# Kernel tuning notes

Hardware: AMD Instinct MI355X
Metric: run time of the kernel (lower is better)

Reference implementation:

```python
import jax, jax.numpy as jnp
import numpy as np
from functools import partial

B, DIN, H, D, HW = 4096, 2048, 1024, 256, 256
MAX_STEPS = 15
STEP = 1.0 / MAX_STEPS
WEIGHT = 1.0


def safe_norm(x):
    # per-sample L2 norm, keepdims, nan-safe at 0
    return jnp.sqrt(jnp.sum(x * x, axis=-1, keepdims=True) + 1e-24)


def setup_inputs() -> dict:
    key = jax.random.key(0)
    ks = jax.random.split(key, 16)
    s = lambda fan: 1.0 / np.sqrt(fan)
    inp = {
        'x_start': jax.random.normal(ks[0], (B, DIN), jnp.float32),
        'x_end': jax.random.normal(ks[1], (B, DIN), jnp.float32),
        'noise_raw': jax.random.normal(ks[2], (B, D), jnp.float32),
        # encoder params
        'W1': jax.random.normal(ks[3], (DIN, H), jnp.float32) * s(DIN),
        'b1': jnp.zeros((H,), jnp.float32),
        'W2': jax.random.normal(ks[4], (H, D), jnp.float32) * s(H),
        'b2': jnp.zeros((D,), jnp.float32),
        # Zermelo wind field params
        'Ww1': jax.random.normal(ks[5], (D, HW), jnp.float32) * s(D),
        'bw1': jnp.zeros((HW,), jnp.float32),
        'Ww2': jax.random.normal(ks[6], (HW, D), jnp.float32) * s(HW),
        'bw2': jnp.zeros((D,), jnp.float32),
        # conformal potential phi params (metric g = exp(phi) I)
        'Wp1': jax.random.normal(ks[7], (D, HW), jnp.float32) * s(D),
        'bp1': jnp.zeros((HW,), jnp.float32),
        'wp2': jax.random.normal(ks[8], (HW,), jnp.float32) * s(HW),
    }
    return inp


def _encode(x, W1, b1, W2, b2):
    return jnp.tanh(x @ W1 + b1) @ W2 + b2  # [B, D]


def _wind(z, Ww1, bw1, Ww2, bw2):
    return jnp.tanh(z @ Ww1 + bw1) @ Ww2 + bw2  # [B, D]


def _grad_phi(x, Wp1, bp1, wp2):
    # phi(x) = wp2 . tanh(x @ Wp1 + bp1); analytic gradient, fully vectorized
    h = jnp.tanh(x @ Wp1 + bp1)          # [B, HW]
    return ((1.0 - h * h) * wp2) @ Wp1.T  # [B, D]


def _accel(x, v, Wp1, bp1, wp2):
    # geodesic spray of conformal metric e^{phi} I:
    # a = -(grad_phi . v) v + 0.5 |v|^2 grad_phi
    g = _grad_phi(x, Wp1, bp1, wp2)
    gv = jnp.sum(g * v, axis=-1, keepdims=True)
    vv = jnp.sum(v * v, axis=-1, keepdims=True)
    return -gv * v + 0.5 * vv * g


def _trace(z0, v0, Wp1, bp1, wp2):
    h = STEP
    acc = partial(_accel, Wp1=Wp1, bp1=bp1, wp2=wp2)

    def step(carry, _):
        x, v = carry
        k1x, k1v = v, acc(x, v)
        k2x, k2v = v + 0.5 * h * k1v, acc(x + 0.5 * h * k1x, v + 0.5 * h * k1v)
        k3x, k3v = v + 0.5 * h * k2v, acc(x + 0.5 * h * k2x, v + 0.5 * h * k2v)
        k4x, k4v = v + h * k3v, acc(x + h * k3x, v + h * k3v)
        xn = x + (h / 6.0) * (k1x + 2 * k2x + 2 * k3x + k4x)
        vn = v + (h / 6.0) * (k1v + 2 * k2v + 2 * k3v + k4v)
        return (xn, vn), xn

    (_, _), xs = jax.lax.scan(step, (z0, v0), None, length=MAX_STEPS)
    return xs  # [MAX_STEPS, B, D] == xs[1:] of the original trace


def reference(x_start, x_end, noise_raw, W1, b1, W2, b2,
              Ww1, bw1, Ww2, bw2, Wp1, bp1, wp2):
    z_s = _encode(x_start, W1, b1, W2, b2)
    z_e = _encode(x_end, W1, b1, W2, b2)
    W_start = _wind(z_s, Ww1, bw1, Ww2, bw2)
    # degenerate-wind fallback: tiny tangent noise (Euclidean manifold -> identity projection)
    noise = noise_raw / (safe_norm(noise_raw) + 1e-12) * 1e-4
    w_norm = safe_norm(W_start)  # [B, 1]
    W_start = jnp.where(w_norm < 1e-5, W_start + noise, W_start)
    xs = _trace(z_s, W_start, Wp1, bp1, wp2)          # [S, B, D]
    dists_sq = jnp.sum((xs - z_e) ** 2, axis=-1)      # [S, B]
    min_dist_sq = jnp.min(dists_sq, axis=0)           # closest approach per sample
    return jnp.mean(min_dist_sq) * WEIGHT
```

## Files before the change

kernel.cpp:

```cpp
#include <hip/hip_runtime.h>
#include <math.h>

typedef short bf8 __attribute__((ext_vector_type(8)));
typedef float f32x4 __attribute__((ext_vector_type(4)));

namespace {

constexpr float H_STEP = 1.0f / 15.0f;

__device__ inline short f2bf(float f) {
  unsigned u = __float_as_uint(f);
  u += 0x7fffu + ((u >> 16) & 1u);
  return (short)(u >> 16);
}

__device__ inline float fast_tanh(float x) {
  const float ax = fabsf(x);
  const float e = __expf(-2.0f * ax);
  const float t = (1.0f - e) * __builtin_amdgcn_rcpf(1.0f + e);
  return copysignf(t, x);
}

__device__ inline float sech2(float x) {
  const float e = __expf(-2.0f * fabsf(x));
  const float r = __builtin_amdgcn_rcpf(1.0f + e);
  return 4.0f * e * r * r;
}

__device__ inline float wave_sum(float v) {
#pragma unroll
  for (int sh = 32; sh > 0; sh >>= 1) v += __shfl_xor(v, sh);
  return v;
}

template <int CTRL>
__device__ inline float dppadd(float v) {
  return v + __int_as_float(__builtin_amdgcn_update_dpp(
                 0, __float_as_int(v), CTRL, 0xF, 0xF, true));
}
__device__ inline float red16(float v) {
  v = dppadd<0x121>(v);
  v = dppadd<0x122>(v);
  v = dppadd<0x124>(v);
  v = dppadd<0x128>(v);
  return v;
}

__device__ inline void async16(const void* g, void* l) {
  __builtin_amdgcn_global_load_lds((__attribute__((address_space(1))) void*)g,
                                   (__attribute__((address_space(3))) void*)l,
                                   16, 0, 0);
}

__global__ __launch_bounds__(256) void prep_all(
    const float* __restrict__ xs, const float* __restrict__ xe,
    const float* __restrict__ W1, const float* __restrict__ W2,
    const float* __restrict__ Ww1, const float* __restrict__ Ww2,
    const float* __restrict__ Wp1, const float* __restrict__ wp2,
    short* __restrict__ XSb, short* __restrict__ W1T, short* __restrict__ W2T,
    short* __restrict__ Ww1T, short* __restrict__ Ww2T,
    short* __restrict__ WpT, short* __restrict__ Wp1s) {
  __shared__ float tile[32][33];
  const int id = blockIdx.x;
  if (id < 2048) {
    const long n = (long)8192 * 2048, half = n >> 1;
    long i = ((long)id * 256 + threadIdx.x) * 4;
    const long stride = (long)2048 * 1024;
    for (; i < n; i += stride) {
      const float* s = (i < half) ? (xs + i) : (xe + (i - half));
      const float4 f = *(const float4*)s;
      ushort4 o;
      o.x = (unsigned short)f2bf(f.x);
      o.y = (unsigned short)f2bf(f.y);
      o.z = (unsigned short)f2bf(f.z);
      o.w = (unsigned short)f2bf(f.w);
      *(ushort4*)(XSb + i) = o;
    }
    return;
  }
  const int tr = threadIdx.x >> 5, tc = threadIdx.x & 31;
  const float* src;
  short* dst;
  int K, N, kt, nt;
  if (id < 4096) {
    src = W1; dst = W1T; K = 2048; N = 1024; kt = (id - 2048) >> 5; nt = (id - 2048) & 31;
  } else if (id < 4352) {
    src = W2; dst = W2T; K = 1024; N = 256; kt = (id - 4096) >> 3; nt = (id - 4096) & 7;
  } else if (id < 4416) {
    src = Ww1; dst = Ww1T; K = 256; N = 256; kt = (id - 4352) >> 3; nt = (id - 4352) & 7;
  } else if (id < 4480) {
    src = Ww2; dst = Ww2T; K = 256; N = 256; kt = (id - 4416) >> 3; nt = (id - 4416) & 7;
  } else if (id < 4544) {
    src = Wp1; dst = WpT; K = 256; N = 256; kt = (id - 4480) >> 3; nt = (id - 4480) & 7;
  } else {
    const int lid = id - 4544;
    const int k0 = (lid >> 3) * 32, n0 = (lid & 7) * 32;
#pragma unroll
    for (int i = 0; i < 32; i += 8) {
      const size_t o = (size_t)(k0 + tr + i) * 256 + n0 + tc;
      Wp1s[o] = f2bf(Wp1[o] * wp2[n0 + tc]);
    }
    return;
  }
  const int k0 = kt * 32, n0 = nt * 32;
#pragma unroll
  for (int i = 0; i < 32; i += 8)
    tile[tr + i][tc] = src[(size_t)(k0 + tr + i) * N + n0 + tc];
  __syncthreads();
#pragma unroll
  for (int i = 0; i < 32; i += 8)
    dst[(size_t)(n0 + tr + i) * K + k0 + tc] = f2bf(tile[tc][tr + i]);
}


__global__ __launch_bounds__(256) void gemm128_tanh(
    const short* __restrict__ A, const short* __restrict__ Bt,
    const float* __restrict__ bias, short* __restrict__ Cb, int M, int N,
    int K) {
  __shared__ __align__(16) short As[2 * 128 * 32];
  __shared__ __align__(16) short Bs[2 * 128 * 32];
  const int tid = threadIdx.x;
  const int w = tid >> 6, lane = tid & 63, q = lane >> 4, l15 = lane & 15;
  const int wm = (w >> 1) * 64, wn = (w & 1) * 64;
  const int m0 = blockIdx.y * 128, n0 = blockIdx.x * 128;
  const f32x4 fzero = {0.0f, 0.0f, 0.0f, 0.0f};
  f32x4 acc[4][4];
#pragma unroll
  for (int mt = 0; mt < 4; ++mt)
#pragma unroll
    for (int nt = 0; nt < 4; ++nt) acc[mt][nt] = fzero;

  for (int k0 = 0; k0 < K; k0 += 64) {
#pragma unroll
    for (int kcb = 0; kcb < 2; ++kcb)
#pragma unroll
      for (int j = 0; j < 2; ++j) {
        const int c = w * 128 + j * 64 + lane;
        async16(A + (size_t)(m0 + (c >> 2)) * K + k0 + kcb * 32 + (c & 3) * 8,
                &As[kcb * 4096 + (w * 128 + j * 64) * 8]);
        async16(Bt + (size_t)(n0 + (c >> 2)) * K + k0 + kcb * 32 + (c & 3) * 8,
                &Bs[kcb * 4096 + (w * 128 + j * 64) * 8]);
      }
    __syncthreads();
#pragma unroll
    for (int kcb = 0; kcb < 2; ++kcb) {
      bf8 af[4], bfr[4];
#pragma unroll
      for (int mt = 0; mt < 4; ++mt)
        af[mt] =
            *(const bf8*)&As[kcb * 4096 + (wm + mt * 16 + l15) * 32 + q * 8];
#pragma unroll
      for (int nt = 0; nt < 4; ++nt)
        bfr[nt] =
            *(const bf8*)&Bs[kcb * 4096 + (wn + nt * 16 + l15) * 32 + q * 8];
#pragma unroll
      for (int mt = 0; mt < 4; ++mt)
#pragma unroll
        for (int nt = 0; nt < 4; ++nt)
          acc[mt][nt] = __builtin_amdgcn_mfma_f32_16x16x32_bf16(
              af[mt], bfr[nt], acc[mt][nt], 0, 0, 0);
    }
    __syncthreads();
  }
#pragma unroll
  for (int mt = 0; mt < 4; ++mt)
#pragma unroll
    for (int nt = 0; nt < 4; ++nt) {
      const int col = n0 + wn + nt * 16 + l15;
      const float bcol = bias[col];
#pragma unroll
      for (int rg = 0; rg < 4; ++rg) {
        const int row = m0 + wm + mt * 16 + q * 4 + rg;
        Cb[(size_t)row * N + col] = f2bf(fast_tanh(acc[mt][nt][rg] + bcol));
      }
    }
}

__global__ __launch_bounds__(256) void gemm64_enc2(
    const short* __restrict__ A, const short* __restrict__ Bt,
    const float* __restrict__ bias, float* __restrict__ Zs,
    float* __restrict__ Ze, int M, int N, int K) {
  __shared__ __align__(16) short As[2 * 64 * 32];
  __shared__ __align__(16) short Bs[2 * 64 * 32];
  const int tid = threadIdx.x;
  const int w = tid >> 6, lane = tid & 63, q = lane >> 4, l15 = lane & 15;
  const int wm = (w >> 1) * 32, wn = (w & 1) * 32;
  const int m0 = blockIdx.y * 64, n0 = blockIdx.x * 64;
  const f32x4 fzero = {0.0f, 0.0f, 0.0f, 0.0f};
  f32x4 acc[2][2];
#pragma unroll
  for (int mt = 0; mt < 2; ++mt)
#pragma unroll
    for (int nt = 0; nt < 2; ++nt) acc[mt][nt] = fzero;

  for (int k0 = 0; k0 < K; k0 += 64) {
    const int c = w * 64 + lane;
#pragma unroll
    for (int kcb = 0; kcb < 2; ++kcb) {
      async16(A + (size_t)(m0 + (c >> 2)) * K + k0 + kcb * 32 + (c & 3) * 8,
              &As[kcb * 2048 + (w * 64) * 8]);
      async16(Bt + (size_t)(n0 + (c >> 2)) * K + k0 + kcb * 32 + (c & 3) * 8,
              &Bs[kcb * 2048 + (w * 64) * 8]);
    }
    __syncthreads();
#pragma unroll
    for (int kcb = 0; kcb < 2; ++kcb) {
      bf8 af[2], bfr[2];
#pragma unroll
      for (int mt = 0; mt < 2; ++mt)
        af[mt] =
            *(const bf8*)&As[kcb * 2048 + (wm + mt * 16 + l15) * 32 + q * 8];
#pragma unroll
      for (int nt = 0; nt < 2; ++nt)
        bfr[nt] =
            *(const bf8*)&Bs[kcb * 2048 + (wn + nt * 16 + l15) * 32 + q * 8];
#pragma unroll
      for (int mt = 0; mt < 2; ++mt)
#pragma unroll
        for (int nt = 0; nt < 2; ++nt)
          acc[mt][nt] = __builtin_amdgcn_mfma_f32_16x16x32_bf16(
              af[mt], bfr[nt], acc[mt][nt], 0, 0, 0);
    }
    __syncthreads();
  }
#pragma unroll
  for (int mt = 0; mt < 2; ++mt)
#pragma unroll
    for (int nt = 0; nt < 2; ++nt) {
      const int col = n0 + wn + nt * 16 + l15;
      const float bcol = bias[col];
#pragma unroll
      for (int rg = 0; rg < 4; ++rg) {
        const int row = m0 + wm + mt * 16 + q * 4 + rg;
        const float val = acc[mt][nt][rg] + bcol;
        if (row < 4096)
          Zs[(size_t)row * N + col] = val;
        else
          Ze[(size_t)(row - 4096) * N + col] = val;
      }
    }
}


__global__ __launch_bounds__(512, 2) void trace_fused(
    const float* __restrict__ Xg, const float* __restrict__ ZEg,
    const float* __restrict__ NZg, const short* __restrict__ WT,
    const short* __restrict__ Wp1s, const short* __restrict__ Ww1T,
    const short* __restrict__ Ww2T, const float* __restrict__ bw1,
    const float* __restrict__ bw2, const float* __restrict__ bp1,
    float* __restrict__ out) {
  constexpr float hs = H_STEP;
  __shared__ __align__(16) short XsL[4096];
  __shared__ __align__(16) short UL[4096];
  __shared__ __align__(16) float gvb[2][16];
  __shared__ __align__(16) float vvb[2][16];
  __shared__ __align__(16) float db[2][16];
  const int tid = threadIdx.x;
  const int w = tid >> 6, lane = tid & 63, q = lane >> 4, l15 = lane & 15;
  const int r0 = blockIdx.x * 16, rb = q * 4;

  if (tid < 16) {
    gvb[0][tid] = 0.0f; gvb[1][tid] = 0.0f;
    vvb[0][tid] = 0.0f; vvb[1][tid] = 0.0f;
    db[0][tid] = 0.0f;  db[1][tid] = 0.0f;
  }

  int cc[2], wadr[2][4], radr[8];
  float bp1c[2], bw1c[2], bw2c[2];
#pragma unroll
  for (int t = 0; t < 2; ++t) {
    const int c = w * 32 + t * 16 + l15;
    cc[t] = c;
    const int kc = c >> 3, cx = kc & 15, cl = c & 7;
#pragma unroll
    for (int rg = 0; rg < 4; ++rg)
      wadr[t][rg] = kc * 128 + ((rb + rg) ^ cx) * 8 + cl;
    bp1c[t] = bp1[c];
    bw1c[t] = bw1[c];
    bw2c[t] = bw2[c];
  }
#pragma unroll
  for (int ks = 0; ks < 8; ++ks) {
    const int kq = ks * 4 + q;
    radr[ks] = (kq * 16 + (l15 ^ (kq & 15))) * 8;
  }
  float x[2][4], ze[2][4], nz[2][4];
#pragma unroll
  for (int t = 0; t < 2; ++t)
#pragma unroll
    for (int rg = 0; rg < 4; ++rg) {
      const size_t off = (size_t)(r0 + rb + rg) * 256 + cc[t];
      x[t][rg] = Xg[off];
      ze[t][rg] = ZEg[off];
      nz[t][rg] = NZg[off];
    }
  const f32x4 fzero = {0.0f, 0.0f, 0.0f, 0.0f};

  float v[2][4];
  {
    bf8 Wf1[2][8], Wf2[2][8];
#pragma unroll
    for (int t = 0; t < 2; ++t)
#pragma unroll
      for (int ks = 0; ks < 8; ++ks) {
        Wf1[t][ks] = *(const bf8*)(Ww1T + cc[t] * 256 + ks * 32 + q * 8);
        Wf2[t][ks] = *(const bf8*)(Ww2T + cc[t] * 256 + ks * 32 + q * 8);
      }
#pragma unroll
    for (int t = 0; t < 2; ++t)
#pragma unroll
      for (int rg = 0; rg < 4; ++rg) XsL[wadr[t][rg]] = f2bf(x[t][rg]);
    __syncthreads();
    bf8 af[8];
#pragma unroll
    for (int ks = 0; ks < 8; ++ks) af[ks] = *(const bf8*)&XsL[radr[ks]];
    f32x4 acc[2];
#pragma unroll
    for (int t = 0; t < 2; ++t) {
      f32x4 a0 = fzero, a1 = fzero;
#pragma unroll
      for (int ks = 0; ks < 8; ks += 2) {
        a0 = __builtin_amdgcn_mfma_f32_16x16x32_bf16(af[ks], Wf1[t][ks], a0,
                                                     0, 0, 0);
        a1 = __builtin_amdgcn_mfma_f32_16x16x32_bf16(af[ks + 1],
                                                     Wf1[t][ks + 1], a1, 0, 0,
                                                     0);
      }
      acc[t] = a0 + a1;
    }
#pragma unroll
    for (int t = 0; t < 2; ++t)
#pragma unroll
      for (int rg = 0; rg < 4; ++rg)
        UL[wadr[t][rg]] = f2bf(fast_tanh(acc[t][rg] + bw1c[t]));
    __syncthreads();
#pragma unroll
    for (int ks = 0; ks < 8; ++ks) af[ks] = *(const bf8*)&UL[radr[ks]];
#pragma unroll
    for (int t = 0; t < 2; ++t) {
      f32x4 a0 = fzero, a1 = fzero;
#pragma unroll
      for (int ks = 0; ks < 8; ks += 2) {
        a0 = __builtin_amdgcn_mfma_f32_16x16x32_bf16(af[ks], Wf2[t][ks], a0,
                                                     0, 0, 0);
        a1 = __builtin_amdgcn_mfma_f32_16x16x32_bf16(af[ks + 1],
                                                     Wf2[t][ks + 1], a1, 0, 0,
                                                     0);
      }
      acc[t] = a0 + a1;
#pragma unroll
      for (int rg = 0; rg < 4; ++rg) v[t][rg] = acc[t][rg] + bw2c[t];
    }
    float pn[4], pm[4];
#pragma unroll
    for (int rg = 0; rg < 4; ++rg) {
      pn[rg] = red16(v[0][rg] * v[0][rg] + v[1][rg] * v[1][rg]);
      pm[rg] = red16(nz[0][rg] * nz[0][rg] + nz[1][rg] * nz[1][rg]);
    }
    if (l15 == 0) {
#pragma unroll
      for (int rg = 0; rg < 4; ++rg) {
        atomicAdd(&gvb[0][rb + rg], pn[rg]);
        atomicAdd(&vvb[0][rb + rg], pm[rg]);
      }
    }
    __syncthreads();
#pragma unroll
    for (int rg = 0; rg < 4; ++rg) {
      const float wn = sqrtf(gvb[0][rb + rg] + 1e-24f);
      const float sc = (wn < 1e-5f)
                           ? 1e-4f / (sqrtf(vvb[0][rb + rg] + 1e-24f) + 1e-12f)
                           : 0.0f;
      v[0][rg] = fmaf(sc, nz[0][rg], v[0][rg]);
      v[1][rg] = fmaf(sc, nz[1][rg], v[1][rg]);
    }
    __syncthreads();
    if (tid < 16) {
      gvb[0][tid] = 0.0f;
      vvb[0][tid] = 0.0f;
    }
    __syncthreads();
  }

  bf8 B1f[2][8], B2f[2][8];
#pragma unroll
  for (int t = 0; t < 2; ++t)
#pragma unroll
    for (int ks = 0; ks < 8; ++ks) {
      B1f[t][ks] = *(const bf8*)(WT + cc[t] * 256 + ks * 32 + q * 8);
      B2f[t][ks] = *(const bf8*)(Wp1s + cc[t] * 256 + ks * 32 + q * 8);
    }
  float ap[2][4], xacc[2][4], vacc[2][4], md[4];
#pragma unroll
  for (int rg = 0; rg < 4; ++rg) {
    ap[0][rg] = 0.0f; ap[1][rg] = 0.0f;
    xacc[0][rg] = 0.0f; xacc[1][rg] = 0.0f;
    vacc[0][rg] = 0.0f; vacc[1][rg] = 0.0f;
    md[rg] = 3.4e38f;
  }
  const float cxv_t[4] = {0.0f, 0.5f * hs, 0.5f * hs, hs};
  const float cxa_t[4] = {0.0f, 0.0f, 0.25f * hs * hs, 0.5f * hs * hs};
  const float cva_t[4] = {0.0f, 0.5f * hs, 0.5f * hs, hs};

#pragma unroll 1
  for (int step = 0; step < 15; ++step) {
#pragma unroll
    for (int st = 0; st < 4; ++st) {
      const int p = st & 1;
      const float cxv = cxv_t[st], cxa = cxa_t[st], cva = cva_t[st];
      float vs[2][4];
#pragma unroll
      for (int t = 0; t < 2; ++t)
#pragma unroll
        for (int rg = 0; rg < 4; ++rg) {
          vs[t][rg] = fmaf(cva, ap[t][rg], v[t][rg]);
          XsL[wadr[t][rg]] =
              f2bf(x[t][rg] + cxv * v[t][rg] + cxa * ap[t][rg]);
        }
      {
        float pv[4];
#pragma unroll
        for (int rg = 0; rg < 4; ++rg)
          pv[rg] = red16(fmaf(vs[0][rg], vs[0][rg], vs[1][rg] * vs[1][rg]));
        if (l15 == 0) {
#pragma unroll
          for (int rg = 0; rg < 4; ++rg) atomicAdd(&vvb[p][rb + rg], pv[rg]);
        }
      }
      __syncthreads();
      if (st == 0 && step > 0) {
        const f32x4 d4 = *(const f32x4*)&db[(step - 1) & 1][rb];
#pragma unroll
        for (int rg = 0; rg < 4; ++rg) md[rg] = fminf(md[rg], d4[rg]);
      }
      bf8 af[8];
#pragma unroll
      for (int ks = 0; ks < 8; ++ks) af[ks] = *(const bf8*)&XsL[radr[ks]];
      f32x4 acc[2];
#pragma unroll
      for (int t = 0; t < 2; ++t) {
        f32x4 a0 = fzero, a1 = fzero;
#pragma unroll
        for (int ks = 0; ks < 8; ks += 2) {
          a0 = __builtin_amdgcn_mfma_f32_16x16x32_bf16(af[ks], B1f[t][ks], a0,
                                                       0, 0, 0);
          a1 = __builtin_amdgcn_mfma_f32_16x16x32_bf16(af[ks + 1],
                                                       B1f[t][ks + 1], a1, 0,
                                                       0, 0);
        }
        acc[t] = a0 + a1;
      }
#pragma unroll
      for (int t = 0; t < 2; ++t)
#pragma unroll
        for (int rg = 0; rg < 4; ++rg)
          UL[wadr[t][rg]] = f2bf(sech2(acc[t][rg] + bp1c[t]));
      if (tid < 16) {
        gvb[p ^ 1][tid] = 0.0f;
        vvb[p ^ 1][tid] = 0.0f;
      }
      __syncthreads();
      if (st == 0 && step > 0 && tid < 16) db[(step - 1) & 1][tid] = 0.0f;
#pragma unroll
      for (int ks = 0; ks < 8; ++ks) af[ks] = *(const bf8*)&UL[radr[ks]];
#pragma unroll
      for (int t = 0; t < 2; ++t) {
        f32x4 a0 = fzero, a1 = fzero;
#pragma unroll
        for (int ks = 0; ks < 8; ks += 2) {
          a0 = __builtin_amdgcn_mfma_f32_16x16x32_bf16(af[ks], B2f[t][ks], a0,
                                                       0, 0, 0);
          a1 = __builtin_amdgcn_mfma_f32_16x16x32_bf16(af[ks + 1],
                                                       B2f[t][ks + 1], a1, 0,
                                                       0, 0);
        }
        acc[t] = a0 + a1;
      }
      {
        float pg[4];
#pragma unroll
        for (int rg = 0; rg < 4; ++rg)
          pg[rg] =
              red16(fmaf(acc[0][rg], vs[0][rg], acc[1][rg] * vs[1][rg]));
        if (l15 == 0) {
#pragma unroll
          for (int rg = 0; rg < 4; ++rg) atomicAdd(&gvb[p][rb + rg], pg[rg]);
        }
      }
      __syncthreads();
      const f32x4 gv4 = *(const f32x4*)&gvb[p][rb];
      const f32x4 vv4 = *(const f32x4*)&vvb[p][rb];
#pragma unroll
      for (int t = 0; t < 2; ++t)
#pragma unroll
        for (int rg = 0; rg < 4; ++rg) {
          const float a = -gv4[rg] * vs[t][rg] + 0.5f * vv4[rg] * acc[t][rg];
          ap[t][rg] = a;
          if (st == 0) {
            xacc[t][rg] = a;
            vacc[t][rg] = a;
          } else if (st < 3) {
            xacc[t][rg] += a;
            vacc[t][rg] += 2.0f * a;
          } else {
            vacc[t][rg] += a;
          }
        }
      if (st == 3) {
        const int sp = step & 1;
        float pd[4];
#pragma unroll
        for (int rg = 0; rg < 4; ++rg) {
          float acc_d = 0.0f;
#pragma unroll
          for (int t = 0; t < 2; ++t) {
            const float xn =
                x[t][rg] + hs * v[t][rg] + (hs * hs / 6.0f) * xacc[t][rg];
            const float vn = v[t][rg] + (hs / 6.0f) * vacc[t][rg];
            x[t][rg] = xn;
            v[t][rg] = vn;
            const float d = xn - ze[t][rg];
            acc_d = fmaf(d, d, acc_d);
          }
          pd[rg] = red16(acc_d);
        }
        if (l15 == 0) {
#pragma unroll
          for (int rg = 0; rg < 4; ++rg) atomicAdd(&db[sp][rb + rg], pd[rg]);
        }
      }
    }
  }
  __syncthreads();
  {
    const f32x4 d4 = *(const f32x4*)&db[14 & 1][rb];
#pragma unroll
    for (int rg = 0; rg < 4; ++rg) md[rg] = fminf(md[rg], d4[rg]);
  }
  if (w == 0 && l15 == 0)
    atomicAdd(out, (md[0] + md[1] + md[2] + md[3]) * (1.0f / 4096.0f));
}

}

extern "C" void kernel_launch(void* const* d_in, const int* in_sizes, int n_in,
                              void* d_out, int out_size, void* d_ws,
                              size_t ws_size, hipStream_t stream) {
  (void)in_sizes; (void)n_in; (void)out_size; (void)ws_size;
  const float* x_start = (const float*)d_in[0];
  const float* x_end = (const float*)d_in[1];
  const float* noise = (const float*)d_in[2];
  const float* W1 = (const float*)d_in[3];
  const float* b1 = (const float*)d_in[4];
  const float* W2 = (const float*)d_in[5];
  const float* b2 = (const float*)d_in[6];
  const float* Ww1 = (const float*)d_in[7];
  const float* bw1 = (const float*)d_in[8];
  const float* Ww2 = (const float*)d_in[9];
  const float* bw2 = (const float*)d_in[10];
  const float* Wp1 = (const float*)d_in[11];
  const float* bp1 = (const float*)d_in[12];
  const float* wp2 = (const float*)d_in[13];
  float* out = (float*)d_out;

  float* Xf = (float*)d_ws;
  float* ZEf = Xf + (size_t)4096 * 256;
  short* XSb = (short*)(ZEf + (size_t)4096 * 256);
  short* H1b = XSb + (size_t)8192 * 2048;
  short* W1T = H1b + (size_t)8192 * 1024;
  short* W2T = W1T + (size_t)1024 * 2048;
  short* Ww1T = W2T + (size_t)256 * 1024;
  short* Ww2T = Ww1T + 65536;
  short* WpT = Ww2T + 65536;
  short* Wp1s = WpT + 65536;

  const dim3 blk(256);

  prep_all<<<4608, blk, 0, stream>>>(x_start, x_end, W1, W2, Ww1, Ww2, Wp1,
                                     wp2, XSb, W1T, W2T, Ww1T, Ww2T, WpT,
                                     Wp1s);
  gemm128_tanh<<<dim3(8, 64), blk, 0, stream>>>(XSb, W1T, b1, H1b, 8192, 1024,
                                                2048);
  gemm64_enc2<<<dim3(4, 128), blk, 0, stream>>>(H1b, W2T, b2, Xf, ZEf, 8192,
                                                256, 1024);
  hipMemsetAsync(d_out, 0, sizeof(float), stream);
  trace_fused<<<256, dim3(512), 0, stream>>>(Xf, ZEf, noise, WpT, Wp1s, Ww1T,
                                             Ww2T, bw1, bw2, bp1, out);
}
```

Baseline: 326.5 us.

## Transpose MFMA operands in trace kernel so each lane owns one row's columns

```diff
diff --git a/kernel.cpp b/kernel.cpp
--- a/kernel.cpp
+++ b/kernel.cpp
@@ -2,6 +2,7 @@
 #include <math.h>
 
 typedef short bf8 __attribute__((ext_vector_type(8)));
+typedef short s4v __attribute__((ext_vector_type(4)));
 typedef float f32x4 __attribute__((ext_vector_type(4)));
 
 namespace {
@@ -25,12 +26,6 @@
   const float e = __expf(-2.0f * fabsf(x));
   const float r = __builtin_amdgcn_rcpf(1.0f + e);
   return 4.0f * e * r * r;
-}
-
-__device__ inline float wave_sum(float v) {
-#pragma unroll
-  for (int sh = 32; sh > 0; sh >>= 1) v += __shfl_xor(v, sh);
-  return v;
 }
 
 template <int CTRL>
@@ -50,6 +45,16 @@
   __builtin_amdgcn_global_load_lds((__attribute__((address_space(1))) void*)g,
                                    (__attribute__((address_space(3))) void*)l,
                                    16, 0, 0);
+}
+
+__device__ inline void stpk4(short* base, int byteoff, float a, float b,
+                             float c, float d) {
+  s4v s;
+  s[0] = f2bf(a);
+  s[1] = f2bf(b);
+  s[2] = f2bf(c);
+  s[3] = f2bf(d);
+  *(s4v*)((char*)base + byteoff) = s;
 }
 
 __global__ __launch_bounds__(256) void prep_all(
@@ -59,10 +64,12 @@
     const float* __restrict__ Wp1, const float* __restrict__ wp2,
     short* __restrict__ XSb, short* __restrict__ W1T, short* __restrict__ W2T,
     short* __restrict__ Ww1T, short* __restrict__ Ww2T,
-    short* __restrict__ WpT, short* __restrict__ Wp1s) {
+    short* __restrict__ WpT, short* __restrict__ Wp1s,
+    float* __restrict__ outz) {
   __shared__ float tile[32][33];
   const int id = blockIdx.x;
   if (id < 2048) {
+    if (id == 0 && threadIdx.x == 0) *outz = 0.0f;
     const long n = (long)8192 * 2048, half = n >> 1;
     long i = ((long)id * 256 + threadIdx.x) * 4;
     const long stride = (long)2048 * 1024;
@@ -252,48 +259,49 @@
   constexpr float hs = H_STEP;
   __shared__ __align__(16) short XsL[4096];
   __shared__ __align__(16) short UL[4096];
-  __shared__ __align__(16) float gvb[2][16];
-  __shared__ __align__(16) float vvb[2][16];
+  __shared__ __align__(16) float gvv[2][16][2];
   __shared__ __align__(16) float db[2][16];
   const int tid = threadIdx.x;
   const int w = tid >> 6, lane = tid & 63, q = lane >> 4, l15 = lane & 15;
-  const int r0 = blockIdx.x * 16, rb = q * 4;
+  const int r0 = blockIdx.x * 16;
+  const int col0 = w * 32 + q * 4;
+  const int wrow = w * 32 + l15;
 
   if (tid < 16) {
-    gvb[0][tid] = 0.0f; gvb[1][tid] = 0.0f;
-    vvb[0][tid] = 0.0f; vvb[1][tid] = 0.0f;
-    db[0][tid] = 0.0f;  db[1][tid] = 0.0f;
-  }
-
-  int cc[2], wadr[2][4], radr[8];
-  float bp1c[2], bw1c[2], bw2c[2];
+    *(float2*)gvv[0][tid] = make_float2(0.f, 0.f);
+    *(float2*)gvv[1][tid] = make_float2(0.f, 0.f);
+    db[0][tid] = 0.f;
+    db[1][tid] = 0.f;
+  }
+
+  const int smask = ((l15 & 7) << 2) ^ (l15 & 3);
+  int wadrT[2], radrT[8];
 #pragma unroll
   for (int t = 0; t < 2; ++t) {
-    const int c = w * 32 + t * 16 + l15;
-    cc[t] = c;
-    const int kc = c >> 3, cx = kc & 15, cl = c & 7;
-#pragma unroll
-    for (int rg = 0; rg < 4; ++rg)
-      wadr[t][rg] = kc * 128 + ((rb + rg) ^ cx) * 8 + cl;
-    bp1c[t] = bp1[c];
-    bw1c[t] = bw1[c];
-    bw2c[t] = bw2[c];
-  }
-#pragma unroll
-  for (int ks = 0; ks < 8; ++ks) {
-    const int kq = ks * 4 + q;
-    radr[ks] = (kq * 16 + (l15 ^ (kq & 15))) * 8;
-  }
+    const int slot = w * 4 + t * 2 + (q >> 1);
+    wadrT[t] = (l15 * 32 + (slot ^ smask)) * 16 + (q & 1) * 8;
+  }
+#pragma unroll
+  for (int ks = 0; ks < 8; ++ks)
+    radrT[ks] = (l15 * 32 + ((ks * 4 + q) ^ smask)) * 16;
+
   float x[2][4], ze[2][4], nz[2][4];
 #pragma unroll
-  for (int t = 0; t < 2; ++t)
-#pragma unroll
-    for (int rg = 0; rg < 4; ++rg) {
-      const size_t off = (size_t)(r0 + rb + rg) * 256 + cc[t];
-      x[t][rg] = Xg[off];
-      ze[t][rg] = ZEg[off];
-      nz[t][rg] = NZg[off];
-    }
+  for (int t = 0; t < 2; ++t) {
+    const size_t off = (size_t)(r0 + l15) * 256 + col0 + t * 16;
+    const float4 xa = *(const float4*)(Xg + off);
+    const float4 za = *(const float4*)(ZEg + off);
+    const float4 na = *(const float4*)(NZg + off);
+    x[t][0] = xa.x; x[t][1] = xa.y; x[t][2] = xa.z; x[t][3] = xa.w;
+    ze[t][0] = za.x; ze[t][1] = za.y; ze[t][2] = za.z; ze[t][3] = za.w;
+    nz[t][0] = na.x; nz[t][1] = na.y; nz[t][2] = na.z; nz[t][3] = na.w;
+  }
+  float bp1c[2][4];
+#pragma unroll
+  for (int t = 0; t < 2; ++t) {
+    const float4 pa = *(const float4*)(bp1 + col0 + t * 16);
+    bp1c[t][0] = pa.x; bp1c[t][1] = pa.y; bp1c[t][2] = pa.z; bp1c[t][3] = pa.w;
+  }
   const f32x4 fzero = {0.0f, 0.0f, 0.0f, 0.0f};
 
   float v[2][4];
@@ -303,82 +311,90 @@
     for (int t = 0; t < 2; ++t)
 #pragma unroll
       for (int ks = 0; ks < 8; ++ks) {
-        Wf1[t][ks] = *(const bf8*)(Ww1T + cc[t] * 256 + ks * 32 + q * 8);
-        Wf2[t][ks] = *(const bf8*)(Ww2T + cc[t] * 256 + ks * 32 + q * 8);
-      }
+        Wf1[t][ks] =
+            *(const bf8*)(Ww1T + (size_t)(wrow + t * 16) * 256 + ks * 32 + q * 8);
+        Wf2[t][ks] =
+            *(const bf8*)(Ww2T + (size_t)(wrow + t * 16) * 256 + ks * 32 + q * 8);
+      }
+    float bw1c[2][4], bw2c[2][4];
+#pragma unroll
+    for (int t = 0; t < 2; ++t) {
+      const float4 a1 = *(const float4*)(bw1 + col0 + t * 16);
+      const float4 a2 = *(const float4*)(bw2 + col0 + t * 16);
+      bw1c[t][0] = a1.x; bw1c[t][1] = a1.y; bw1c[t][2] = a1.z; bw1c[t][3] = a1.w;
+      bw2c[t][0] = a2.x; bw2c[t][1] = a2.y; bw2c[t][2] = a2.z; bw2c[t][3] = a2.w;
+    }
 #pragma unroll
     for (int t = 0; t < 2; ++t)
-#pragma unroll
-      for (int rg = 0; rg < 4; ++rg) XsL[wadr[t][rg]] = f2bf(x[t][rg]);
+      stpk4(XsL, wadrT[t], x[t][0], x[t][1], x[t][2], x[t][3]);
     __syncthreads();
     bf8 af[8];
 #pragma unroll
-    for (int ks = 0; ks < 8; ++ks) af[ks] = *(const bf8*)&XsL[radr[ks]];
+    for (int ks = 0; ks < 8; ++ks)
+      af[ks] = *(const bf8*)((const char*)XsL + radrT[ks]);
     f32x4 acc[2];
 #pragma unroll
     for (int t = 0; t < 2; ++t) {
       f32x4 a0 = fzero, a1 = fzero;
 #pragma unroll
       for (int ks = 0; ks < 8; ks += 2) {
-        a0 = __builtin_amdgcn_mfma_f32_16x16x32_bf16(af[ks], Wf1[t][ks], a0,
-                                                     0, 0, 0);
-        a1 = __builtin_amdgcn_mfma_f32_16x16x32_bf16(af[ks + 1],
-                                                     Wf1[t][ks + 1], a1, 0, 0,
-                                                     0);
+        a0 = __builtin_amdgcn_mfma_f32_16x16x32_bf16(Wf1[t][ks], af[ks], a0, 0,
+                                                     0, 0);
+        a1 = __builtin_amdgcn_mfma_f32_16x16x32_bf16(Wf1[t][ks + 1],
+                                                     af[ks + 1], a1, 0, 0, 0);
       }
       acc[t] = a0 + a1;
     }
 #pragma unroll
     for (int t = 0; t < 2; ++t)
-#pragma unroll
-      for (int rg = 0; rg < 4; ++rg)
-        UL[wadr[t][rg]] = f2bf(fast_tanh(acc[t][rg] + bw1c[t]));
-    __syncthreads();
-#pragma unroll
-    for (int ks = 0; ks < 8; ++ks) af[ks] = *(const bf8*)&UL[radr[ks]];
+      stpk4(UL, wadrT[t], fast_tanh(acc[t][0] + bw1c[t][0]),
+            fast_tanh(acc[t][1] + bw1c[t][1]),
+            fast_tanh(acc[t][2] + bw1c[t][2]),
+            fast_tanh(acc[t][3] + bw1c[t][3]));
+    __syncthreads();
+#pragma unroll
+    for (int ks = 0; ks < 8; ++ks)
+      af[ks] = *(const bf8*)((const char*)UL + radrT[ks]);
 #pragma unroll
     for (int t = 0; t < 2; ++t) {
       f32x4 a0 = fzero, a1 = fzero;
 #pragma unroll
       for (int ks = 0; ks < 8; ks += 2) {
-        a0 = __builtin_amdgcn_mfma_f32_16x16x32_bf16(af[ks], Wf2[t][ks], a0,
-                                                     0, 0, 0);
-        a1 = __builtin_amdgcn_mfma_f32_16x16x32_bf16(af[ks + 1],
-                                                     Wf2[t][ks + 1], a1, 0, 0,
-                                                     0);
+        a0 = __builtin_amdgcn_mfma_f32_16x16x32_bf16(Wf2[t][ks], af[ks], a0, 0,
+                                                     0, 0);
+        a1 = __builtin_amdgcn_mfma_f32_16x16x32_bf16(Wf2[t][ks + 1],
+                                                     af[ks + 1], a1, 0, 0, 0);
       }
       acc[t] = a0 + a1;
 #pragma unroll
-      for (int rg = 0; rg < 4; ++rg) v[t][rg] = acc[t][rg] + bw2c[t];
-    }
-    float pn[4], pm[4];
-#pragma unroll
-    for (int rg = 0; rg < 4; ++rg) {
-      pn[rg] = red16(v[0][rg] * v[0][rg] + v[1][rg] * v[1][rg]);
-      pm[rg] = red16(nz[0][rg] * nz[0][rg] + nz[1][rg] * nz[1][rg]);
-    }
-    if (l15 == 0) {
+      for (int rg = 0; rg < 4; ++rg) v[t][rg] = acc[t][rg] + bw2c[t][rg];
+    }
+    float pn = 0.f, pm = 0.f;
+#pragma unroll
+    for (int t = 0; t < 2; ++t)
 #pragma unroll
       for (int rg = 0; rg < 4; ++rg) {
-        atomicAdd(&gvb[0][rb + rg], pn[rg]);
-        atomicAdd(&vvb[0][rb + rg], pm[rg]);
-      }
-    }
-    __syncthreads();
-#pragma unroll
-    for (int rg = 0; rg < 4; ++rg) {
-      const float wn = sqrtf(gvb[0][rb + rg] + 1e-24f);
-      const float sc = (wn < 1e-5f)
-                           ? 1e-4f / (sqrtf(vvb[0][rb + rg] + 1e-24f) + 1e-12f)
-                           : 0.0f;
-      v[0][rg] = fmaf(sc, nz[0][rg], v[0][rg]);
-      v[1][rg] = fmaf(sc, nz[1][rg], v[1][rg]);
-    }
-    __syncthreads();
-    if (tid < 16) {
-      gvb[0][tid] = 0.0f;
-      vvb[0][tid] = 0.0f;
-    }
+        pn = fmaf(v[t][rg], v[t][rg], pn);
+        pm = fmaf(nz[t][rg], nz[t][rg], pm);
+      }
+    pn += __shfl_xor(pn, 16);
+    pn += __shfl_xor(pn, 32);
+    pm += __shfl_xor(pm, 16);
+    pm += __shfl_xor(pm, 32);
+    if (q == 0) {
+      atomicAdd(&gvv[0][l15][0], pn);
+      atomicAdd(&gvv[0][l15][1], pm);
+    }
+    __syncthreads();
+    const float wn = sqrtf(gvv[0][l15][0] + 1e-24f);
+    const float sc =
+        (wn < 1e-5f) ? 1e-4f / (sqrtf(gvv[0][l15][1] + 1e-24f) + 1e-12f) : 0.0f;
+#pragma unroll
+    for (int t = 0; t < 2; ++t)
+#pragma unroll
+      for (int rg = 0; rg < 4; ++rg) v[t][rg] = fmaf(sc, nz[t][rg], v[t][rg]);
+    __syncthreads();
+    if (tid < 16) *(float2*)gvv[0][tid] = make_float2(0.f, 0.f);
     __syncthreads();
   }
 
@@ -387,17 +403,17 @@
   for (int t = 0; t < 2; ++t)
 #pragma unroll
     for (int ks = 0; ks < 8; ++ks) {
-      B1f[t][ks] = *(const bf8*)(WT + cc[t] * 256 + ks * 32 + q * 8);
-      B2f[t][ks] = *(const bf8*)(Wp1s + cc[t] * 256 + ks * 32 + q * 8);
-    }
-  float ap[2][4], xacc[2][4], vacc[2][4], md[4];
-#pragma unroll
-  for (int rg = 0; rg < 4; ++rg) {
-    ap[0][rg] = 0.0f; ap[1][rg] = 0.0f;
-    xacc[0][rg] = 0.0f; xacc[1][rg] = 0.0f;
-    vacc[0][rg] = 0.0f; vacc[1][rg] = 0.0f;
-    md[rg] = 3.4e38f;
-  }
+      B1f[t][ks] =
+          *(const bf8*)(WT + (size_t)(wrow + t * 16) * 256 + ks * 32 + q * 8);
+      B2f[t][ks] =
+          *(const bf8*)(Wp1s + (size_t)(wrow + t * 16) * 256 + ks * 32 + q * 8);
+    }
+  float ap[2][4], xacc[2][4], vacc[2][4];
+#pragma unroll
+  for (int t = 0; t < 2; ++t)
+#pragma unroll
+    for (int rg = 0; rg < 4; ++rg) ap[t][rg] = 0.0f;
+  float md = 3.4e38f;
   const float cxv_t[4] = {0.0f, 0.5f * hs, 0.5f * hs, hs};
   const float cxa_t[4] = {0.0f, 0.0f, 0.25f * hs * hs, 0.5f * hs * hs};
   const float cva_t[4] = {0.0f, 0.5f * hs, 0.5f * hs, hs};
@@ -408,93 +424,79 @@
     for (int st = 0; st < 4; ++st) {
       const int p = st & 1;
       const float cxv = cxv_t[st], cxa = cxa_t[st], cva = cva_t[st];
-      float vs[2][4];
-#pragma unroll
-      for (int t = 0; t < 2; ++t)
+      float vs[2][4], pv = 0.f;
+#pragma unroll
+      for (int t = 0; t < 2; ++t) {
+        float sx[4];
 #pragma unroll
         for (int rg = 0; rg < 4; ++rg) {
           vs[t][rg] = fmaf(cva, ap[t][rg], v[t][rg]);
-          XsL[wadr[t][rg]] =
-              f2bf(x[t][rg] + cxv * v[t][rg] + cxa * ap[t][rg]);
+          sx[rg] = x[t][rg] + cxv * v[t][rg] + cxa * ap[t][rg];
+          pv = fmaf(vs[t][rg], vs[t][rg], pv);
         }
-      {
-        float pv[4];
-#pragma unroll
-        for (int rg = 0; rg < 4; ++rg)
-          pv[rg] = red16(fmaf(vs[0][rg], vs[0][rg], vs[1][rg] * vs[1][rg]));
-        if (l15 == 0) {
-#pragma unroll
-          for (int rg = 0; rg < 4; ++rg) atomicAdd(&vvb[p][rb + rg], pv[rg]);
-        }
-      }
+        stpk4(XsL, wadrT[t], sx[0], sx[1], sx[2], sx[3]);
+      }
+      pv += __shfl_xor(pv, 16);
+      pv += __shfl_xor(pv, 32);
+      if (q == 0) atomicAdd(&gvv[p][l15][1], pv);
       __syncthreads();
-      if (st == 0 && step > 0) {
-        const f32x4 d4 = *(const f32x4*)&db[(step - 1) & 1][rb];
-#pragma unroll
-        for (int rg = 0; rg < 4; ++rg) md[rg] = fminf(md[rg], d4[rg]);
-      }
+      if (st == 0 && step > 0) md = fminf(md, db[(step - 1) & 1][l15]);
       bf8 af[8];
 #pragma unroll
-      for (int ks = 0; ks < 8; ++ks) af[ks] = *(const bf8*)&XsL[radr[ks]];
+      for (int ks = 0; ks < 8; ++ks)
+        af[ks] = *(const bf8*)((const char*)XsL + radrT[ks]);
       f32x4 acc[2];
 #pragma unroll
       for (int t = 0; t < 2; ++t) {
         f32x4 a0 = fzero, a1 = fzero;
 #pragma unroll
         for (int ks = 0; ks < 8; ks += 2) {
-          a0 = __builtin_amdgcn_mfma_f32_16x16x32_bf16(af[ks], B1f[t][ks], a0,
+          a0 = __builtin_amdgcn_mfma_f32_16x16x32_bf16(B1f[t][ks], af[ks], a0,
                                                        0, 0, 0);
-          a1 = __builtin_amdgcn_mfma_f32_16x16x32_bf16(af[ks + 1],
-                                                       B1f[t][ks + 1], a1, 0,
-                                                       0, 0);
+          a1 = __builtin_amdgcn_mfma_f32_16x16x32_bf16(B1f[t][ks + 1],
+                                                       af[ks + 1], a1, 0, 0,
+                                                       0);
         }
         acc[t] = a0 + a1;
-      }
-#pragma unroll
-      for (int t = 0; t < 2; ++t)
-#pragma unroll
-        for (int rg = 0; rg < 4; ++rg)
-          UL[wadr[t][rg]] = f2bf(sech2(acc[t][rg] + bp1c[t]));
-      if (tid < 16) {
-        gvb[p ^ 1][tid] = 0.0f;
-        vvb[p ^ 1][tid] = 0.0f;
-      }
+        stpk4(UL, wadrT[t], sech2(acc[t][0] + bp1c[t][0]),
+              sech2(acc[t][1] + bp1c[t][1]), sech2(acc[t][2] + bp1c[t][2]),
+              sech2(acc[t][3] + bp1c[t][3]));
+      }
+      if (tid < 16) *(float2*)gvv[p ^ 1][tid] = make_float2(0.f, 0.f);
       __syncthreads();
       if (st == 0 && step > 0 && tid < 16) db[(step - 1) & 1][tid] = 0.0f;
 #pragma unroll
-      for (int ks = 0; ks < 8; ++ks) af[ks] = *(const bf8*)&UL[radr[ks]];
+      for (int ks = 0; ks < 8; ++ks)
+        af[ks] = *(const bf8*)((const char*)UL + radrT[ks]);
 #pragma unroll
       for (int t = 0; t < 2; ++t) {
         f32x4 a0 = fzero, a1 = fzero;
 #pragma unroll
         for (int ks = 0; ks < 8; ks += 2) {
-          a0 = __builtin_amdgcn_mfma_f32_16x16x32_bf16(af[ks], B2f[t][ks], a0,
+          a0 = __builtin_amdgcn_mfma_f32_16x16x32_bf16(B2f[t][ks], af[ks], a0,
                                                        0, 0, 0);
-          a1 = __builtin_amdgcn_mfma_f32_16x16x32_bf16(af[ks + 1],
-                                                       B2f[t][ks + 1], a1, 0,
-                                                       0, 0);
+          a1 = __builtin_amdgcn_mfma_f32_16x16x32_bf16(B2f[t][ks + 1],
+                                                       af[ks + 1], a1, 0, 0,
+                                                       0);
         }
         acc[t] = a0 + a1;
       }
-      {
-        float pg[4];
-#pragma unroll
-        for (int rg = 0; rg < 4; ++rg)
-          pg[rg] =
-              red16(fmaf(acc[0][rg], vs[0][rg], acc[1][rg] * vs[1][rg]));
-        if (l15 == 0) {
-#pragma unroll
-          for (int rg = 0; rg < 4; ++rg) atomicAdd(&gvb[p][rb + rg], pg[rg]);
-        }
-      }
+      float pg = 0.f;
+#pragma unroll
+      for (int t = 0; t < 2; ++t)
+#pragma unroll
+        for (int rg = 0; rg < 4; ++rg) pg = fmaf(acc[t][rg], vs[t][rg], pg);
+      pg += __shfl_xor(pg, 16);
+      pg += __shfl_xor(pg, 32);
+      if (q == 0) atomicAdd(&gvv[p][l15][0], pg);
       __syncthreads();
-      const f32x4 gv4 = *(const f32x4*)&gvb[p][rb];
-      const f32x4 vv4 = *(const f32x4*)&vvb[p][rb];
+      const float2 r2 = *(const float2*)gvv[p][l15];
+      const float gv = r2.x, vv = r2.y;
 #pragma unroll
       for (int t = 0; t < 2; ++t)
 #pragma unroll
         for (int rg = 0; rg < 4; ++rg) {
-          const float a = -gv4[rg] * vs[t][rg] + 0.5f * vv4[rg] * acc[t][rg];
+          const float a = -gv * vs[t][rg] + 0.5f * vv * acc[t][rg];
           ap[t][rg] = a;
           if (st == 0) {
             xacc[t][rg] = a;
@@ -508,37 +510,31 @@
         }
       if (st == 3) {
         const int sp = step & 1;
-        float pd[4];
-#pragma unroll
-        for (int rg = 0; rg < 4; ++rg) {
-          float acc_d = 0.0f;
-#pragma unroll
-          for (int t = 0; t < 2; ++t) {
+        float pd = 0.f;
+#pragma unroll
+        for (int t = 0; t < 2; ++t)
+#pragma unroll
+          for (int rg = 0; rg < 4; ++rg) {
             const float xn =
                 x[t][rg] + hs * v[t][rg] + (hs * hs / 6.0f) * xacc[t][rg];
             const float vn = v[t][rg] + (hs / 6.0f) * vacc[t][rg];
             x[t][rg] = xn;
             v[t][rg] = vn;
-            const float d = xn - ze[t][rg];
-            acc_d = fmaf(d, d, acc_d);
+            const float dd = xn - ze[t][rg];
+            pd = fmaf(dd, dd, pd);
           }
-          pd[rg] = red16(acc_d);
-        }
-        if (l15 == 0) {
-#pragma unroll
-          for (int rg = 0; rg < 4; ++rg) atomicAdd(&db[sp][rb + rg], pd[rg]);
-        }
+        pd += __shfl_xor(pd, 16);
+        pd += __shfl_xor(pd, 32);
+        if (q == 0) atomicAdd(&db[sp][l15], pd);
       }
     }
   }
   __syncthreads();
-  {
-    const f32x4 d4 = *(const f32x4*)&db[14 & 1][rb];
-#pragma unroll
-    for (int rg = 0; rg < 4; ++rg) md[rg] = fminf(md[rg], d4[rg]);
-  }
-  if (w == 0 && l15 == 0)
-    atomicAdd(out, (md[0] + md[1] + md[2] + md[3]) * (1.0f / 4096.0f));
+  md = fminf(md, db[14 & 1][l15]);
+  if (w == 0) {
+    const float s = red16(md);
+    if (tid == 0) atomicAdd(out, s * (1.0f / 4096.0f));
+  }
 }
 
 }
@@ -578,12 +574,11 @@
 
   prep_all<<<4608, blk, 0, stream>>>(x_start, x_end, W1, W2, Ww1, Ww2, Wp1,
                                      wp2, XSb, W1T, W2T, Ww1T, Ww2T, WpT,
-                                     Wp1s);
+                                     Wp1s, out);
   gemm128_tanh<<<dim3(8, 64), blk, 0, stream>>>(XSb, W1T, b1, H1b, 8192, 1024,
                                                 2048);
   gemm64_enc2<<<dim3(4, 128), blk, 0, stream>>>(H1b, W2T, b2, Xf, ZEf, 8192,
                                                 256, 1024);
-  hipMemsetAsync(d_out, 0, sizeof(float), stream);
   trace_fused<<<256, dim3(512), 0, stream>>>(Xf, ZEf, noise, WpT, Wp1s, Ww1T,
                                              Ww2T, bw1, bw2, bp1, out);
 }
```

After: 320.1 us. 2.0% less time.
